# Optimization experiments

Measured on AMD Instinct MI355X. Metric: run time of the kernel, lower is better.

The kernel has to match this reference:

```python
import jax, jax.numpy as jnp
import numpy as np

B, K, N, NBR = 4, 2048, 8192, 32
DIM, C_IN, W_HID, C_MID, F_HID, C_OUT = 3, 16, 32, 16, 64, 64
BIG = 3000.0


def _mlp(x, w1, b1, w2, b2):
    # SetTransform with one hidden layer, reduction='none': Linear->ReLU->Linear
    return jnp.maximum(x @ w1 + b1, 0.0) @ w2 + b2


def setup_inputs() -> dict:
    key = jax.random.key(0)
    ks = jax.random.split(key, 12)
    s = lambda fan_in: 1.0 / np.sqrt(fan_in)
    return {
        "keys": jax.random.normal(ks[0], (B, K, DIM), jnp.float32),
        "points": jax.random.normal(ks[1], (B, N, DIM), jnp.float32),
        "feats": jax.random.normal(ks[2], (B, N, C_IN), jnp.float32),
        "valid": jax.random.bernoulli(ks[3], 0.95, (B, K, N)),
        "ww1": jax.random.normal(ks[4], (DIM, W_HID), jnp.float32) * s(DIM),
        "wb1": jax.random.normal(ks[5], (W_HID,), jnp.float32) * s(DIM),
        "ww2": jax.random.normal(ks[6], (W_HID, C_MID), jnp.float32) * s(W_HID),
        "wb2": jax.random.normal(ks[7], (C_MID,), jnp.float32) * s(W_HID),
        "fw1": jax.random.normal(ks[8], (C_IN * C_MID, F_HID), jnp.float32) * s(C_IN * C_MID),
        "fb1": jax.random.normal(ks[9], (F_HID,), jnp.float32) * s(C_IN * C_MID),
        "fw2": jax.random.normal(ks[10], (F_HID, C_OUT), jnp.float32) * s(F_HID),
        "fb2": jax.random.normal(ks[11], (C_OUT,), jnp.float32) * s(F_HID),
    }


def reference(keys, points, feats, valid, ww1, wb1, ww2, wb2, fw1, fb1, fw2, fb2):
    # --- dist_fn (Euclidean): dist_vec = points - keys, dist = ||dist_vec|| ---
    diff = points[:, None, :, :] - keys[:, :, None, :]        # [B,K,N,DIM]
    dist = jnp.sqrt(jnp.sum(diff * diff, axis=-1))            # [B,K,N]
    big_dist = dist.max() * BIG
    dist = dist + jnp.where(valid, 0.0, big_dist)
    # --- kNN: smallest NBR distances per key ---
    _, idxs = jax.lax.top_k(-dist, NBR)                       # [B,K,NBR]
    bidx = jnp.arange(B)[:, None, None]
    # gather neighbor info (avoids materializing [B,K,N,*] gathered copies)
    n_rel = points[bidx, idxs] - keys[:, :, None, :]          # [B,K,NBR,DIM]
    n_feats = feats[bidx, idxs]                               # [B,K,NBR,C_IN]
    n_valid = jnp.take_along_axis(valid, idxs, axis=2)        # [B,K,NBR]
    n_valid = n_valid[..., None].astype(n_rel.dtype)
    # per-neighbor weight MLP, mask, batched matmul reduce over neighbors
    m = _mlp(n_rel, ww1, wb1, ww2, wb2) * n_valid             # [B,K,NBR,C_MID]
    nf = n_feats * n_valid                                    # [B,K,NBR,C_IN]
    e = jnp.einsum('bkqm,bkqc->bkmc', m, nf)                  # [B,K,C_MID,C_IN]
    e = e.reshape(B, K, C_MID * C_IN)
    return _mlp(e, fw1, fb1, fw2, fb2)                        # [B,K,C_OUT]
```

## Files before the change

kernel.cpp:

```cpp
#include <hip/hip_runtime.h>
#include <hip/hip_bf16.h>
#include <cstdint>
#include <cstddef>

#define B_    4
#define K_    2048
#define N_    8192
#define NBR_  32
#define NCAND 40
#define CIN   16
#define WHID  32
#define CMID  16
#define FHID  64
#define COUT  64

__global__ void pc_detect_kernel(const unsigned* __restrict__ v, int* __restrict__ flag) {
    const unsigned w = v[threadIdx.x & 63];
    const int byte_like = (((w & 0xFEFEFEFEu) == 0u) && ((w & 0xFFFFFF00u) != 0u)) ? 1 : 0;
    const unsigned long long m = __ballot(byte_like);
    if (threadIdx.x == 0) *flag = (m != 0ull) ? 1 : 0;
}

__device__ __forceinline__ unsigned umin_(unsigned a, unsigned b) { return a < b ? a : b; }
__device__ __forceinline__ unsigned umax_(unsigned a, unsigned b) { return a < b ? b : a; }

__device__ __forceinline__ void insert8(unsigned (&sa)[8], unsigned kv) {
    if (kv < sa[7]) {
#pragma unroll
        for (int i = 0; i < 8; ++i) {
            unsigned lo = umin_(sa[i], kv);
            kv = umax_(sa[i], kv);
            sa[i] = lo;
        }
    }
}

template <int BYTE>
__device__ __forceinline__ void scan_pts4(const float* __restrict__ pts,
                                          const void* __restrict__ vpv,
                                          float kx, float ky, float kz,
                                          int lane, unsigned (&sa)[8]) {
#pragma unroll 2
    for (int t = 0; t < N_ / 256; ++t) {
        const int n0 = t * 256 + lane * 4;
        const float4* p4 = (const float4*)(pts + (size_t)n0 * 3);
        const float4 A = p4[0];
        const float4 Bv = p4[1];
        const float4 Cv = p4[2];
        unsigned v0, v1, v2, v3;
        if (BYTE) {
            const unsigned vw = *(const unsigned*)((const unsigned char*)vpv + n0);
            v0 = vw & 0xffu; v1 = vw & 0xff00u; v2 = vw & 0xff0000u; v3 = vw & 0xff000000u;
        } else {
            const uint4 vw = *(const uint4*)((const unsigned*)vpv + n0);
            v0 = vw.x; v1 = vw.y; v2 = vw.z; v3 = vw.w;
        }
        float dx, dy, dz, d2;
        dx = A.x - kx; dy = A.y - ky; dz = A.z - kz;
        d2 = fmaf(dz, dz, fmaf(dy, dy, dx * dx));
        const unsigned kv0 = v0 ? ((__float_as_uint(d2) & 0xFFFFE000u) | (unsigned)(n0 + 0)) : 0xFFFFFFFFu;
        dx = A.w - kx; dy = Bv.x - ky; dz = Bv.y - kz;
        d2 = fmaf(dz, dz, fmaf(dy, dy, dx * dx));
        const unsigned kv1 = v1 ? ((__float_as_uint(d2) & 0xFFFFE000u) | (unsigned)(n0 + 1)) : 0xFFFFFFFFu;
        dx = Bv.z - kx; dy = Bv.w - ky; dz = Cv.x - kz;
        d2 = fmaf(dz, dz, fmaf(dy, dy, dx * dx));
        const unsigned kv2 = v2 ? ((__float_as_uint(d2) & 0xFFFFE000u) | (unsigned)(n0 + 2)) : 0xFFFFFFFFu;
        dx = Cv.y - kx; dy = Cv.z - ky; dz = Cv.w - kz;
        d2 = fmaf(dz, dz, fmaf(dy, dy, dx * dx));
        const unsigned kv3 = v3 ? ((__float_as_uint(d2) & 0xFFFFE000u) | (unsigned)(n0 + 3)) : 0xFFFFFFFFu;
        insert8(sa, kv0);
        insert8(sa, kv1);
        insert8(sa, kv2);
        insert8(sa, kv3);
    }
}

struct Slice {
    union {
        unsigned cand[8 * 64];
        float    w[NBR_ * CMID];
        float    hf_pad[512];
    } A;
    union {
        float nf[NBR_ * CIN];
        struct { float hp[4 * FHID]; float hf[FHID]; } h;
    } Bv;
    union {
        unsigned slot[NBR_];
        float    e[CMID * CIN];
    } C;
};

__global__ __launch_bounds__(256, 6) void pc_main_kernel(
    const float* __restrict__ keys,
    const float* __restrict__ points,
    const float* __restrict__ feats,
    const void*  __restrict__ validp,
    const float* __restrict__ ww1, const float* __restrict__ wb1,
    const float* __restrict__ ww2, const float* __restrict__ wb2,
    const float* __restrict__ fw1, const float* __restrict__ fb1,
    const float* __restrict__ fw2, const float* __restrict__ fb2,
    float* __restrict__ out,
    const int* __restrict__ flagp)
{
    __shared__ Slice sl[4];

    const int lane = threadIdx.x & 63;
    const int wv   = threadIdx.x >> 6;
    const int row  = (blockIdx.x << 2) | wv;
    const int b    = row >> 11;
    Slice& S = sl[wv];

    const float kx = keys[row * 3 + 0];
    const float ky = keys[row * 3 + 1];
    const float kz = keys[row * 3 + 2];
    const float* pts = points + (size_t)b * N_ * 3;
    const int flag = *flagp;

    unsigned sa[8];
#pragma unroll
    for (int i = 0; i < 8; ++i) sa[i] = 0xFFFFFFFFu;

    const size_t vbase = (size_t)row * N_;
    if (flag) {
        scan_pts4<1>(pts, (const void*)((const unsigned char*)validp + vbase), kx, ky, kz, lane, sa);
    } else {
        scan_pts4<0>(pts, (const void*)((const unsigned*)validp + vbase), kx, ky, kz, lane, sa);
    }

#pragma unroll
    for (int i = 0; i < 8; ++i) S.A.cand[i * 64 + lane] = sa[i];
    __syncthreads();

    unsigned cur   = sa[0];
    int      head  = 0;
    unsigned mykey = 0xFFFFFFFFu;
#pragma unroll 4
    for (int r = 0; r < NCAND; ++r) {
        unsigned t = cur;
#pragma unroll
        for (int off = 1; off < 64; off <<= 1)
            t = umin_(t, (unsigned)__shfl_xor((int)t, off, 64));
        if (lane == r) mykey = t;
        if (cur == t) {
            ++head;
            cur = (head < 8) ? S.A.cand[head * 64 + lane] : 0xFFFFFFFFu;
        }
    }

    if (lane < NBR_) S.C.slot[lane] = 0xFFFFFFFFu;
    __syncthreads();

    {
        const bool fin  = (mykey < 0xF0000000u);
        const int  cidx = (int)(mykey & 8191u);
        float cd2 = 3.0e38f;
        if (fin) {
            const float cdx = pts[cidx * 3 + 0] - kx;
            const float cdy = pts[cidx * 3 + 1] - ky;
            const float cdz = pts[cidx * 3 + 2] - kz;
            cd2 = fmaf(cdz, cdz, fmaf(cdy, cdy, cdx * cdx));
        }
        const unsigned long long fkey =
            fin ? (((unsigned long long)__float_as_uint(cd2) << 13) | (unsigned long long)cidx)
                : ~0ull;
        int rank = 0;
#pragma unroll 8
        for (int j = 0; j < NCAND; ++j) {
            const unsigned long long fj = (unsigned long long)__shfl((long long)fkey, j, 64);
            rank += (fj < fkey) ? 1 : 0;
        }
        if (fin && rank < NBR_)
            S.C.slot[rank] = mykey;
    }
    __syncthreads();

    const int q    = lane & 31;
    const int half = lane >> 5;
    const unsigned skey = S.C.slot[q];
    const int   nidx = (int)(skey & 8191u);
    const float vf   = (skey < 0xF0000000u) ? 1.0f : 0.0f;

    const float rx = pts[nidx * 3 + 0] - kx;
    const float ry = pts[nidx * 3 + 1] - ky;
    const float rz = pts[nidx * 3 + 2] - kz;

    float wacc[8];
    {
        const float4 b0 = *(const float4*)&wb2[half * 8 + 0];
        const float4 b1 = *(const float4*)&wb2[half * 8 + 4];
        wacc[0] = b0.x; wacc[1] = b0.y; wacc[2] = b0.z; wacc[3] = b0.w;
        wacc[4] = b1.x; wacc[5] = b1.y; wacc[6] = b1.z; wacc[7] = b1.w;
    }

#pragma unroll 8
    for (int j = 0; j < WHID; ++j) {
        float hj = fmaf(rx, ww1[j], fmaf(ry, ww1[WHID + j], fmaf(rz, ww1[2 * WHID + j], wb1[j])));
        hj = fmaxf(hj, 0.0f);
        const float4 wa = *(const float4*)&ww2[j * CMID + half * 8 + 0];
        const float4 wb = *(const float4*)&ww2[j * CMID + half * 8 + 4];
        wacc[0] = fmaf(hj, wa.x, wacc[0]);
        wacc[1] = fmaf(hj, wa.y, wacc[1]);
        wacc[2] = fmaf(hj, wa.z, wacc[2]);
        wacc[3] = fmaf(hj, wa.w, wacc[3]);
        wacc[4] = fmaf(hj, wb.x, wacc[4]);
        wacc[5] = fmaf(hj, wb.y, wacc[5]);
        wacc[6] = fmaf(hj, wb.z, wacc[6]);
        wacc[7] = fmaf(hj, wb.w, wacc[7]);
    }
#pragma unroll
    for (int m = 0; m < 8; ++m) wacc[m] *= vf;

    *(float4*)&S.A.w[q * CMID + half * 8 + 0] = make_float4(wacc[0], wacc[1], wacc[2], wacc[3]);
    *(float4*)&S.A.w[q * CMID + half * 8 + 4] = make_float4(wacc[4], wacc[5], wacc[6], wacc[7]);

    const float* fp = feats + ((size_t)b * N_ + (size_t)nidx) * CIN + half * 8;
    *(float4*)&S.Bv.nf[q * CIN + half * 8 + 0] = *(const float4*)(fp + 0);
    *(float4*)&S.Bv.nf[q * CIN + half * 8 + 4] = *(const float4*)(fp + 4);
    __syncthreads();

    {
        const int m  = lane >> 2;
        const int c4 = lane & 3;
        float4 eacc = make_float4(0.f, 0.f, 0.f, 0.f);
#pragma unroll
        for (int qq = 0; qq < NBR_; ++qq) {
            const float  wq = S.A.w[qq * CMID + m];
            const float4 f  = *(const float4*)&S.Bv.nf[qq * CIN + c4 * 4];
            eacc.x = fmaf(wq, f.x, eacc.x);
            eacc.y = fmaf(wq, f.y, eacc.y);
            eacc.z = fmaf(wq, f.z, eacc.z);
            eacc.w = fmaf(wq, f.w, eacc.w);
        }
        *(float4*)&S.C.e[m * CIN + c4 * 4] = eacc;
    }
    __syncthreads();

    {
        const int g  = lane >> 4;
        const int t4 = lane & 15;
        float a0 = 0.f, a1 = 0.f, a2 = 0.f, a3 = 0.f;
#pragma unroll 8
        for (int i = 0; i < 64; ++i) {
            const float  ev = S.C.e[g * 64 + i];
            const float4 wv2 = *(const float4*)&fw1[(size_t)(g * 64 + i) * FHID + t4 * 4];
            a0 = fmaf(ev, wv2.x, a0);
            a1 = fmaf(ev, wv2.y, a1);
            a2 = fmaf(ev, wv2.z, a2);
            a3 = fmaf(ev, wv2.w, a3);
        }
        *(float4*)&S.Bv.h.hp[g * FHID + t4 * 4] = make_float4(a0, a1, a2, a3);
    }
    __syncthreads();

    {
        float hf = fb1[lane] + S.Bv.h.hp[lane] + S.Bv.h.hp[FHID + lane]
                 + S.Bv.h.hp[2 * FHID + lane] + S.Bv.h.hp[3 * FHID + lane];
        S.Bv.h.hf[lane] = fmaxf(hf, 0.0f);
    }
    __syncthreads();

    {
        float oacc = fb2[lane];
#pragma unroll 8
        for (int j = 0; j < FHID; ++j)
            oacc = fmaf(S.Bv.h.hf[j], fw2[(size_t)j * COUT + lane], oacc);
        out[(size_t)row * COUT + lane] = oacc;
    }
}

extern "C" void kernel_launch(void* const* d_in, const int* in_sizes, int n_in,
                              void* d_out, int out_size, void* d_ws, size_t ws_size,
                              hipStream_t stream) {
    const float* keys   = (const float*)d_in[0];
    const float* points = (const float*)d_in[1];
    const float* feats  = (const float*)d_in[2];
    const void*  valid  = d_in[3];
    const float* ww1 = (const float*)d_in[4];
    const float* wb1 = (const float*)d_in[5];
    const float* ww2 = (const float*)d_in[6];
    const float* wb2 = (const float*)d_in[7];
    const float* fw1 = (const float*)d_in[8];
    const float* fb1 = (const float*)d_in[9];
    const float* fw2 = (const float*)d_in[10];
    const float* fb2 = (const float*)d_in[11];
    float* out = (float*)d_out;
    int*   flag = (int*)d_ws;

    pc_detect_kernel<<<1, 64, 0, stream>>>((const unsigned*)valid, flag);
    pc_main_kernel<<<(B_ * K_) / 4, 256, 0, stream>>>(keys, points, feats, valid,
                                                      ww1, wb1, ww2, wb2,
                                                      fw1, fb1, fw2, fb2,
                                                      out, flag);
}
```

Before: 444.3 us.

## Pre-pack valid mask into bitmask in a separate kernel before kNN scan

```diff
diff --git a/kernel.cpp b/kernel.cpp
--- a/kernel.cpp
+++ b/kernel.cpp
@@ -13,6 +13,9 @@
 #define CMID  16
 #define FHID  64
 #define COUT  64
+#define PKW   (N_ / 64)
+#define PK_OFF 4096
+#define WS_NEED ((size_t)PK_OFF + (size_t)B_ * K_ * (N_ / 8))
 
 __global__ void pc_detect_kernel(const unsigned* __restrict__ v, int* __restrict__ flag) {
     const unsigned w = v[threadIdx.x & 63];
@@ -21,6 +24,35 @@
     if (threadIdx.x == 0) *flag = (m != 0ull) ? 1 : 0;
 }
 
+__global__ __launch_bounds__(256) void pc_pack_kernel(
+    const void* __restrict__ vin, unsigned long long* __restrict__ pk,
+    const int* __restrict__ flagp)
+{
+    const int lane = threadIdx.x & 63;
+    const int wv   = threadIdx.x >> 6;
+    const int row  = (blockIdx.x << 2) | wv;
+    const size_t base = (size_t)row * N_;
+    unsigned long long* prow = pk + (size_t)row * PKW;
+    const int flag = *flagp;
+    if (flag) {
+        const unsigned char* vp = (const unsigned char*)vin + base;
+#pragma unroll 8
+        for (int i = 0; i < PKW; ++i) {
+            const unsigned char bb = vp[i * 64 + lane];
+            const unsigned long long m = __ballot(bb != 0);
+            if (lane == 0) prow[i] = m;
+        }
+    } else {
+        const unsigned* vp = (const unsigned*)vin + base;
+#pragma unroll 8
+        for (int i = 0; i < PKW; ++i) {
+            const unsigned vv = vp[i * 64 + lane];
+            const unsigned long long m = __ballot(vv != 0);
+            if (lane == 0) prow[i] = m;
+        }
+    }
+}
+
 __device__ __forceinline__ unsigned umin_(unsigned a, unsigned b) { return a < b ? a : b; }
 __device__ __forceinline__ unsigned umax_(unsigned a, unsigned b) { return a < b ? b : a; }
 
@@ -32,6 +64,41 @@
             kv = umax_(sa[i], kv);
             sa[i] = lo;
         }
+    }
+}
+
+
+__device__ __forceinline__ void scan_pts4_packed(const float* __restrict__ pts,
+                                                 const unsigned* __restrict__ pkrow32,
+                                                 float kx, float ky, float kz,
+                                                 int lane, unsigned (&sa)[8]) {
+    const unsigned shift = (unsigned)(lane & 7) * 4u;
+    const unsigned* pw = pkrow32 + (lane >> 3);
+#pragma unroll 4
+    for (int t = 0; t < N_ / 256; ++t) {
+        const int n0 = t * 256 + lane * 4;
+        const float4* p4 = (const float4*)(pts + (size_t)n0 * 3);
+        const float4 A  = p4[0];
+        const float4 Bv = p4[1];
+        const float4 Cv = p4[2];
+        const unsigned nib = pw[t * 8] >> shift;
+        float dx, dy, dz, d2;
+        dx = A.x - kx; dy = A.y - ky; dz = A.z - kz;
+        d2 = fmaf(dz, dz, fmaf(dy, dy, dx * dx));
+        const unsigned kv0 = (nib & 1u) ? ((__float_as_uint(d2) & 0xFFFFE000u) | (unsigned)(n0 + 0)) : 0xFFFFFFFFu;
+        dx = A.w - kx; dy = Bv.x - ky; dz = Bv.y - kz;
+        d2 = fmaf(dz, dz, fmaf(dy, dy, dx * dx));
+        const unsigned kv1 = (nib & 2u) ? ((__float_as_uint(d2) & 0xFFFFE000u) | (unsigned)(n0 + 1)) : 0xFFFFFFFFu;
+        dx = Bv.z - kx; dy = Bv.w - ky; dz = Cv.x - kz;
+        d2 = fmaf(dz, dz, fmaf(dy, dy, dx * dx));
+        const unsigned kv2 = (nib & 4u) ? ((__float_as_uint(d2) & 0xFFFFE000u) | (unsigned)(n0 + 2)) : 0xFFFFFFFFu;
+        dx = Cv.y - kx; dy = Cv.z - ky; dz = Cv.w - kz;
+        d2 = fmaf(dz, dz, fmaf(dy, dy, dx * dx));
+        const unsigned kv3 = (nib & 8u) ? ((__float_as_uint(d2) & 0xFFFFE000u) | (unsigned)(n0 + 3)) : 0xFFFFFFFFu;
+        insert8(sa, kv0);
+        insert8(sa, kv1);
+        insert8(sa, kv2);
+        insert8(sa, kv3);
     }
 }
 
@@ -44,7 +111,7 @@
     for (int t = 0; t < N_ / 256; ++t) {
         const int n0 = t * 256 + lane * 4;
         const float4* p4 = (const float4*)(pts + (size_t)n0 * 3);
-        const float4 A = p4[0];
+        const float4 A  = p4[0];
         const float4 Bv = p4[1];
         const float4 Cv = p4[2];
         unsigned v0, v1, v2, v3;
@@ -79,7 +146,7 @@
     union {
         unsigned cand[8 * 64];
         float    w[NBR_ * CMID];
-        float    hf_pad[512];
+        float    pad_[512];
     } A;
     union {
         float nf[NBR_ * CIN];
@@ -91,11 +158,13 @@
     } C;
 };
 
-__global__ __launch_bounds__(256, 6) void pc_main_kernel(
+template <int PACKED>
+__global__ __launch_bounds__(256, 8) void pc_main_kernel(
     const float* __restrict__ keys,
     const float* __restrict__ points,
     const float* __restrict__ feats,
     const void*  __restrict__ validp,
+    const unsigned* __restrict__ pk32,
     const float* __restrict__ ww1, const float* __restrict__ wb1,
     const float* __restrict__ ww2, const float* __restrict__ wb2,
     const float* __restrict__ fw1, const float* __restrict__ fb1,
@@ -115,17 +184,21 @@
     const float ky = keys[row * 3 + 1];
     const float kz = keys[row * 3 + 2];
     const float* pts = points + (size_t)b * N_ * 3;
-    const int flag = *flagp;
 
     unsigned sa[8];
 #pragma unroll
     for (int i = 0; i < 8; ++i) sa[i] = 0xFFFFFFFFu;
 
-    const size_t vbase = (size_t)row * N_;
-    if (flag) {
-        scan_pts4<1>(pts, (const void*)((const unsigned char*)validp + vbase), kx, ky, kz, lane, sa);
+    if (PACKED) {
+        scan_pts4_packed(pts, pk32 + (size_t)row * (PKW * 2), kx, ky, kz, lane, sa);
     } else {
-        scan_pts4<0>(pts, (const void*)((const unsigned*)validp + vbase), kx, ky, kz, lane, sa);
+        const int flag = *flagp;
+        const size_t vbase = (size_t)row * N_;
+        if (flag) {
+            scan_pts4<1>(pts, (const void*)((const unsigned char*)validp + vbase), kx, ky, kz, lane, sa);
+        } else {
+            scan_pts4<0>(pts, (const void*)((const unsigned*)validp + vbase), kx, ky, kz, lane, sa);
+        }
     }
 
 #pragma unroll
@@ -286,10 +359,18 @@
     const float* fb2 = (const float*)d_in[11];
     float* out = (float*)d_out;
     int*   flag = (int*)d_ws;
+    unsigned long long* pk = (unsigned long long*)((char*)d_ws + PK_OFF);
 
     pc_detect_kernel<<<1, 64, 0, stream>>>((const unsigned*)valid, flag);
-    pc_main_kernel<<<(B_ * K_) / 4, 256, 0, stream>>>(keys, points, feats, valid,
-                                                      ww1, wb1, ww2, wb2,
-                                                      fw1, fb1, fw2, fb2,
-                                                      out, flag);
-}
+
+    if (ws_size >= WS_NEED) {
+        pc_pack_kernel<<<(B_ * K_) / 4, 256, 0, stream>>>(valid, pk, flag);
+        pc_main_kernel<1><<<(B_ * K_) / 4, 256, 0, stream>>>(
+            keys, points, feats, valid, (const unsigned*)pk,
+            ww1, wb1, ww2, wb2, fw1, fb1, fw2, fb2, out, flag);
+    } else {
+        pc_main_kernel<0><<<(B_ * K_) / 4, 256, 0, stream>>>(
+            keys, points, feats, valid, (const unsigned*)pk,
+            ww1, wb1, ww2, wb2, fw1, fb1, fw2, fb2, out, flag);
+    }
+}
```

After: 516.9 us. +16.4%, slower.
